# Kernel tuning notes

Hardware: AMD Instinct MI355X
Metric: run time of the kernel (lower is better)

The kernel has to match this reference:

```python
import jax, jax.numpy as jnp
import numpy as np

N_NODES = 50000
N_EDGES = 600000
D_IN, D_HID, D_OUT = 128, 256, 128


def setup_inputs() -> dict:
    key = jax.random.key(0)
    ks = jax.random.split(key, 8)
    x = jax.random.normal(ks[0], (N_NODES, D_IN), dtype=jnp.float32)
    edge_index = jax.random.randint(ks[1], (2, N_EDGES), 0, N_NODES, dtype=jnp.int64)
    # init_method='uniform' -> edge_weights initialized to ones
    edge_weights = jnp.ones((N_EDGES,), dtype=jnp.float32)
    def lin(k, din, dout):
        s = 1.0 / np.sqrt(din)
        return jax.random.uniform(k, (din, dout), jnp.float32, -s, s)
    W1 = lin(ks[2], D_IN, D_HID)
    b1 = jnp.zeros((D_HID,), jnp.float32)
    W2 = lin(ks[3], D_HID, D_HID)
    b2 = jnp.zeros((D_HID,), jnp.float32)
    W3 = lin(ks[4], D_HID, D_OUT)
    b3 = jnp.zeros((D_OUT,), jnp.float32)
    return {"x": x, "edge_index": edge_index, "edge_weights": edge_weights,
            "W1": W1, "b1": b1, "W2": W2, "b2": b2, "W3": W3, "b3": b3}


def reference(x, edge_index, edge_weights, W1, b1, W2, b2, W3, b3):
    N = x.shape[0]
    # learnable metric: softplus on raw edge weights
    ew = jax.nn.softplus(edge_weights)
    src, dst = edge_index[0], edge_index[1]
    # GCNConv default: add self-loops with weight 1.0
    loop = jnp.arange(N, dtype=edge_index.dtype)
    s = jnp.concatenate([src, loop])
    d = jnp.concatenate([dst, loop])
    w = jnp.concatenate([ew, jnp.ones((N,), ew.dtype)])
    # symmetric degree normalization (gcn_norm); identical edge_weight across layers
    deg = jax.ops.segment_sum(w, d, num_segments=N)
    dinv = jnp.where(deg > 0, jax.lax.rsqrt(deg), jnp.zeros_like(deg))
    norm = dinv[s] * w * dinv[d]  # [E+N]

    def gcn_conv(h, W, b):
        h = h @ W                              # [N, dout]
        msg = h[s] * norm[:, None]             # gather + scale: [E+N, dout]
        out = jax.ops.segment_sum(msg, d, num_segments=N)  # scatter-add
        return out + b

    h = jax.nn.relu(gcn_conv(x, W1, b1))   # dropout p=0.0 -> identity
    h = jax.nn.relu(gcn_conv(h, W2, b2))
    return gcn_conv(h, W3, b3)
```

## Files before the change

kernel.cpp:

```cpp
#include <hip/hip_runtime.h>
#include <hip/hip_fp16.h>
#include <math.h>

#define N_NODES 50000
#define N_EDGES 600000
#define D_IN    128
#define D_HID   256
#define D_OUT   128
#define NB_SCAN ((N_NODES + 255) / 256)

typedef unsigned short u16;
typedef __attribute__((ext_vector_type(8))) _Float16 f16x8;
typedef __attribute__((ext_vector_type(4))) float f32x4;

__device__ __forceinline__ u16 f2h(float x) {
    __half h = __float2half_rn(x);
    return *reinterpret_cast<u16*>(&h);
}
__device__ __forceinline__ float h2f(u16 h) {
    __half hh = *reinterpret_cast<__half*>(&h);
    return __half2float(hh);
}
__device__ __forceinline__ float2 h2f2(unsigned int raw) {
    __half2 h = *reinterpret_cast<__half2*>(&raw);
    return __half22float2(h);
}


__global__ void k_hist(const int* __restrict__ dst, const float* __restrict__ w,
                       float* __restrict__ ew, int* __restrict__ rank,
                       int* __restrict__ cnt) {
    int e = blockIdx.x * blockDim.x + threadIdx.x;
    if (e >= N_EDGES) return;
    float x = w[e];
    ew[e] = fmaxf(x, 0.f) + log1pf(expf(-fabsf(x)));
    rank[e] = atomicAdd(&cnt[dst[e]], 1);
}

__global__ void k_scan1(const int* __restrict__ cnt, int* __restrict__ rowptr,
                        int* __restrict__ bsum) {
    __shared__ int s[256];
    int b = blockIdx.x, t = threadIdx.x;
    int i = b * 256 + t;
    int v = (i < N_NODES) ? cnt[i] : 0;
    s[t] = v;
    __syncthreads();
    for (int off = 1; off < 256; off <<= 1) {
        int u = (t >= off) ? s[t - off] : 0;
        __syncthreads();
        s[t] += u;
        __syncthreads();
    }
    if (i < N_NODES) rowptr[i] = s[t] - v;
    if (t == 255) bsum[b] = s[255];
}

__global__ void k_scan2(const int* __restrict__ bsum, int* __restrict__ boff) {
    __shared__ int s[256];
    int t = threadIdx.x;
    int v = (t < NB_SCAN) ? bsum[t] : 0;
    s[t] = v;
    __syncthreads();
    for (int off = 1; off < 256; off <<= 1) {
        int u = (t >= off) ? s[t - off] : 0;
        __syncthreads();
        s[t] += u;
        __syncthreads();
    }
    if (t < NB_SCAN) boff[t] = s[t] - v;
    if (t == 255) boff[NB_SCAN] = s[255];
}

__global__ void k_scan3(int* __restrict__ rowptr, const int* __restrict__ boff) {
    int b = blockIdx.x, t = threadIdx.x;
    int i = b * 256 + t;
    if (i < N_NODES) rowptr[i] += boff[b];
    if (i == 0) rowptr[N_NODES] = boff[NB_SCAN];
}

__global__ void k_fill2(const int* __restrict__ src, const int* __restrict__ dst,
                        const float* __restrict__ ew, const int* __restrict__ rank,
                        const int* __restrict__ rowptr, int2* __restrict__ ecsr) {
    int e = blockIdx.x * blockDim.x + threadIdx.x;
    if (e >= N_EDGES) return;
    int pos = rowptr[dst[e]] + rank[e];
    ecsr[pos] = make_int2(src[e], __float_as_int(ew[e]));
}

__global__ void k_degdinv(const int* __restrict__ rowptr, const int2* __restrict__ ecsr,
                          float* __restrict__ dinv) {
    int n = blockIdx.x * blockDim.x + threadIdx.x;
    if (n >= N_NODES) return;
    int beg = rowptr[n], end = rowptr[n + 1];
    float s = 1.0f;
    for (int p = beg; p < end; p++) s += __int_as_float(ecsr[p].y);
    dinv[n] = rsqrtf(s);
}

__global__ void k_norm(const int* __restrict__ rowptr, const float* __restrict__ dinv,
                       int2* __restrict__ ecsr) {
    int n = blockIdx.x * blockDim.x + threadIdx.x;
    if (n >= N_NODES) return;
    int beg = rowptr[n], end = rowptr[n + 1];
    float dn = dinv[n];
    for (int p = beg; p < end; p++) {
        int2 r = ecsr[p];
        float w = dinv[r.x] * __int_as_float(r.y) * dn;
        ecsr[p] = make_int2(r.x, __float_as_int(w));
    }
}


#define WPREP_TOTAL 131072

__global__ void k_wprep(const float* __restrict__ W1, const float* __restrict__ W2,
                        const float* __restrict__ W3,
                        u16* __restrict__ B1, u16* __restrict__ B2, u16* __restrict__ B3) {
    int idx = blockIdx.x * blockDim.x + threadIdx.x;
    const float* W; u16* B; int K, N, base;
    if (idx < 32768)       { W = W1; B = B1; K = 128; N = 256; base = 0; }
    else if (idx < 98304)  { W = W2; B = B2; K = 256; N = 256; base = 32768; }
    else if (idx < 131072) { W = W3; B = B3; K = 256; N = 128; base = 98304; }
    else return;
    int p = idx - base;
    int n = p % N, k = p / N;
    float x = W[(size_t)k * N + n];
    u16 hi = f2h(x);
    u16 lo = f2h(x - h2f(hi));
    B[(size_t)n * (2 * K) + k] = hi;
    B[(size_t)n * (2 * K) + K + k] = lo;
}


template <int D, int INF, int OUTM, bool BIAS>
__global__ __launch_bounds__(256) void k_agg(const void* __restrict__ inv,
                                             const int* __restrict__ rowptr,
                                             const int2* __restrict__ ecsr,
                                             const float* __restrict__ dinv,
                                             const float* __restrict__ bias,
                                             void* __restrict__ outv) {
    int node = blockIdx.x * 4 + (threadIdx.x >> 6);
    int lane = threadIdx.x & 63;
    if (node >= N_NODES) return;
    float dn = dinv[node];
    float dd = dn * dn;
    int beg = rowptr[node], end = rowptr[node + 1];

    if (D == 256) {
        const float* inf = (const float*)inv;
        const u16* inh = (const u16*)inv;
        float sx, sy, sz, sw;
        if (INF == 0) {
            float4 sv = *(reinterpret_cast<const float4*>(inf + (size_t)node * D) + lane);
            sx = sv.x; sy = sv.y; sz = sv.z; sw = sv.w;
        } else {
            uint2 raw = *reinterpret_cast<const uint2*>(inh + (size_t)node * D + lane * 4);
            float2 f01 = h2f2(raw.x), f23 = h2f2(raw.y);
            sx = f01.x; sy = f01.y; sz = f23.x; sw = f23.y;
        }
        float ax = dd * sx, ay = dd * sy, az = dd * sz, aw = dd * sw;
        int p = beg;
        for (; p + 4 <= end; p += 4) {
            int2 e0 = ecsr[p], e1 = ecsr[p + 1], e2 = ecsr[p + 2], e3 = ecsr[p + 3];
            float w0 = __int_as_float(e0.y), w1 = __int_as_float(e1.y);
            float w2 = __int_as_float(e2.y), w3 = __int_as_float(e3.y);
            if (INF == 0) {
                float4 r0 = *(reinterpret_cast<const float4*>(inf + (size_t)e0.x * D) + lane);
                float4 r1 = *(reinterpret_cast<const float4*>(inf + (size_t)e1.x * D) + lane);
                float4 r2 = *(reinterpret_cast<const float4*>(inf + (size_t)e2.x * D) + lane);
                float4 r3 = *(reinterpret_cast<const float4*>(inf + (size_t)e3.x * D) + lane);
                ax += w0 * r0.x; ay += w0 * r0.y; az += w0 * r0.z; aw += w0 * r0.w;
                ax += w1 * r1.x; ay += w1 * r1.y; az += w1 * r1.z; aw += w1 * r1.w;
                ax += w2 * r2.x; ay += w2 * r2.y; az += w2 * r2.z; aw += w2 * r2.w;
                ax += w3 * r3.x; ay += w3 * r3.y; az += w3 * r3.z; aw += w3 * r3.w;
            } else {
                uint2 q0 = *reinterpret_cast<const uint2*>(inh + (size_t)e0.x * D + lane * 4);
                uint2 q1 = *reinterpret_cast<const uint2*>(inh + (size_t)e1.x * D + lane * 4);
                uint2 q2 = *reinterpret_cast<const uint2*>(inh + (size_t)e2.x * D + lane * 4);
                uint2 q3 = *reinterpret_cast<const uint2*>(inh + (size_t)e3.x * D + lane * 4);
                float2 a0 = h2f2(q0.x), b0 = h2f2(q0.y);
                float2 a1 = h2f2(q1.x), b1 = h2f2(q1.y);
                float2 a2 = h2f2(q2.x), b2 = h2f2(q2.y);
                float2 a3 = h2f2(q3.x), b3 = h2f2(q3.y);
                ax += w0 * a0.x; ay += w0 * a0.y; az += w0 * b0.x; aw += w0 * b0.y;
                ax += w1 * a1.x; ay += w1 * a1.y; az += w1 * b1.x; aw += w1 * b1.y;
                ax += w2 * a2.x; ay += w2 * a2.y; az += w2 * b2.x; aw += w2 * b2.y;
                ax += w3 * a3.x; ay += w3 * a3.y; az += w3 * b3.x; aw += w3 * b3.y;
            }
        }
        for (; p < end; p++) {
            int2 e0 = ecsr[p];
            float w0 = __int_as_float(e0.y);
            if (INF == 0) {
                float4 r0 = *(reinterpret_cast<const float4*>(inf + (size_t)e0.x * D) + lane);
                ax += w0 * r0.x; ay += w0 * r0.y; az += w0 * r0.z; aw += w0 * r0.w;
            } else {
                uint2 q0 = *reinterpret_cast<const uint2*>(inh + (size_t)e0.x * D + lane * 4);
                float2 a0 = h2f2(q0.x), b0 = h2f2(q0.y);
                ax += w0 * a0.x; ay += w0 * a0.y; az += w0 * b0.x; aw += w0 * b0.y;
            }
        }
        if (OUTM == 0) {
            float* out = (float*)outv;
            if (BIAS) {
                float4 b = *(reinterpret_cast<const float4*>(bias) + lane);
                ax += b.x; ay += b.y; az += b.z; aw += b.w;
            }
            float4 res; res.x = ax; res.y = ay; res.z = az; res.w = aw;
            *(reinterpret_cast<float4*>(out + (size_t)node * D) + lane) = res;
        } else {
            u16* out = (u16*)outv;
            ushort4 hv;
            hv.x = f2h(ax); hv.y = f2h(ay); hv.z = f2h(az); hv.w = f2h(aw);
            *reinterpret_cast<ushort4*>(out + (size_t)node * D + lane * 4) = hv;
        }
    } else {
        const float* inf = (const float*)inv;
        const u16* inh = (const u16*)inv;
        float sx, sy;
        if (INF == 0) {
            float2 sv = *(reinterpret_cast<const float2*>(inf + (size_t)node * D) + lane);
            sx = sv.x; sy = sv.y;
        } else {
            unsigned int raw = *reinterpret_cast<const unsigned int*>(inh + (size_t)node * D + lane * 2);
            float2 f = h2f2(raw);
            sx = f.x; sy = f.y;
        }
        float ax = dd * sx, ay = dd * sy;
        int p = beg;
        for (; p + 4 <= end; p += 4) {
            int2 e0 = ecsr[p], e1 = ecsr[p + 1], e2 = ecsr[p + 2], e3 = ecsr[p + 3];
            float w0 = __int_as_float(e0.y), w1 = __int_as_float(e1.y);
            float w2 = __int_as_float(e2.y), w3 = __int_as_float(e3.y);
            if (INF == 0) {
                float2 r0 = *(reinterpret_cast<const float2*>(inf + (size_t)e0.x * D) + lane);
                float2 r1 = *(reinterpret_cast<const float2*>(inf + (size_t)e1.x * D) + lane);
                float2 r2 = *(reinterpret_cast<const float2*>(inf + (size_t)e2.x * D) + lane);
                float2 r3 = *(reinterpret_cast<const float2*>(inf + (size_t)e3.x * D) + lane);
                ax += w0 * r0.x; ay += w0 * r0.y;
                ax += w1 * r1.x; ay += w1 * r1.y;
                ax += w2 * r2.x; ay += w2 * r2.y;
                ax += w3 * r3.x; ay += w3 * r3.y;
            } else {
                unsigned int q0 = *reinterpret_cast<const unsigned int*>(inh + (size_t)e0.x * D + lane * 2);
                unsigned int q1 = *reinterpret_cast<const unsigned int*>(inh + (size_t)e1.x * D + lane * 2);
                unsigned int q2 = *reinterpret_cast<const unsigned int*>(inh + (size_t)e2.x * D + lane * 2);
                unsigned int q3 = *reinterpret_cast<const unsigned int*>(inh + (size_t)e3.x * D + lane * 2);
                float2 f0 = h2f2(q0), f1 = h2f2(q1), f2 = h2f2(q2), f3 = h2f2(q3);
                ax += w0 * f0.x; ay += w0 * f0.y;
                ax += w1 * f1.x; ay += w1 * f1.y;
                ax += w2 * f2.x; ay += w2 * f2.y;
                ax += w3 * f3.x; ay += w3 * f3.y;
            }
        }
        for (; p < end; p++) {
            int2 e0 = ecsr[p];
            float w0 = __int_as_float(e0.y);
            if (INF == 0) {
                float2 r0 = *(reinterpret_cast<const float2*>(inf + (size_t)e0.x * D) + lane);
                ax += w0 * r0.x; ay += w0 * r0.y;
            } else {
                unsigned int q0 = *reinterpret_cast<const unsigned int*>(inh + (size_t)e0.x * D + lane * 2);
                float2 f0 = h2f2(q0);
                ax += w0 * f0.x; ay += w0 * f0.y;
            }
        }
        if (OUTM == 0) {
            float* out = (float*)outv;
            if (BIAS) {
                float2 b = *(reinterpret_cast<const float2*>(bias) + lane);
                ax += b.x; ay += b.y;
            }
            float2 res; res.x = ax; res.y = ay;
            *(reinterpret_cast<float2*>(out + (size_t)node * D) + lane) = res;
        } else {
            u16* out = (u16*)outv;
            ushort2 hv; hv.x = f2h(ax); hv.y = f2h(ay);
            *reinterpret_cast<ushort2*>(out + (size_t)node * D + lane * 2) = hv;
        }
    }
}


template <int OUT, bool BIAS, bool RELU>
__global__ __launch_bounds__(256) void k_gemm_h(const u16* __restrict__ Ap,
                                                const u16* __restrict__ Bp,
                                                const float* __restrict__ bias,
                                                void* __restrict__ Cv,
                                                int M, int K, int NN) {
    const int KP2 = 2 * K;
    __shared__ u16 As[8 * 544];
    __shared__ u16 Bs[2 * 8 * 544];
    int tid = threadIdx.x;
    int bm = blockIdx.y * 128;
    int bn = blockIdx.x * 128;
    int l = tid & 63;
    int w = tid >> 6;
    int wr = w >> 1, wc = w & 1;

    f32x4 zero = {0.f, 0.f, 0.f, 0.f};
    f32x4 acc[4][4];
    #pragma unroll
    for (int i = 0; i < 4; i++)
        #pragma unroll
        for (int j = 0; j < 4; j++) acc[i][j] = zero;

    for (int k0 = 0; k0 < K; k0 += 32) {
        #pragma unroll
        for (int q = 0; q < 2; q++) {
            int idx = tid + q * 256;
            int r = idx >> 2, o = idx & 3;
            int gr = bm + r;
            uint4 va = make_uint4(0u, 0u, 0u, 0u);
            if (gr < M)
                va = *reinterpret_cast<const uint4*>(Ap + (size_t)gr * K + k0 + o * 8);
            *reinterpret_cast<uint4*>(&As[(r >> 4) * 544 + o * 136 + (r & 15) * 8]) = va;
        }
        #pragma unroll
        for (int q = 0; q < 4; q++) {
            int idx = tid + q * 256;
            int r = idx >> 3, oct = idx & 7;
            int hf = oct >> 2, o = oct & 3;
            uint4 vb = *reinterpret_cast<const uint4*>(
                Bp + (size_t)(bn + r) * KP2 + hf * K + k0 + o * 8);
            *reinterpret_cast<uint4*>(
                &Bs[hf * 4352 + (r >> 4) * 544 + o * 136 + (r & 15) * 8]) = vb;
        }
        __syncthreads();
        int fro = (l >> 4) * 136 + (l & 15) * 8;
        f16x8 a[4], bh[4], bl[4];
        #pragma unroll
        for (int i = 0; i < 4; i++)
            a[i] = *reinterpret_cast<const f16x8*>(&As[(wr * 4 + i) * 544 + fro]);
        #pragma unroll
        for (int j = 0; j < 4; j++) {
            bh[j] = *reinterpret_cast<const f16x8*>(&Bs[(wc * 4 + j) * 544 + fro]);
            bl[j] = *reinterpret_cast<const f16x8*>(&Bs[4352 + (wc * 4 + j) * 544 + fro]);
        }
        #pragma unroll
        for (int i = 0; i < 4; i++)
            #pragma unroll
            for (int j = 0; j < 4; j++) {
                acc[i][j] = __builtin_amdgcn_mfma_f32_16x16x32_f16(a[i], bh[j], acc[i][j], 0, 0, 0);
                acc[i][j] = __builtin_amdgcn_mfma_f32_16x16x32_f16(a[i], bl[j], acc[i][j], 0, 0, 0);
            }
        __syncthreads();
    }

    int cl = l & 15;
    int rq = (l >> 4) * 4;
    float bv[4];
    #pragma unroll
    for (int j = 0; j < 4; j++) {
        int gc = bn + wc * 64 + j * 16 + cl;
        bv[j] = BIAS ? bias[gc] : 0.f;
    }
    #pragma unroll
    for (int i = 0; i < 4; i++) {
        #pragma unroll
        for (int r = 0; r < 4; r++) {
            int grow = bm + wr * 64 + i * 16 + rq + r;
            if (grow >= M) continue;
            #pragma unroll
            for (int j = 0; j < 4; j++) {
                int gc = bn + wc * 64 + j * 16 + cl;
                float v = acc[i][j][r];
                if (BIAS) v += bv[j];
                if (RELU) v = fmaxf(v, 0.f);
                if (OUT == 0) {
                    ((float*)Cv)[(size_t)grow * NN + gc] = v;
                } else {
                    ((u16*)Cv)[(size_t)grow * NN + gc] = f2h(v);
                }
            }
        }
    }
}


extern "C" void kernel_launch(void* const* d_in, const int* in_sizes, int n_in,
                              void* d_out, int out_size, void* d_ws, size_t ws_size,
                              hipStream_t stream) {
    const float* x   = (const float*)d_in[0];
    const int*   ei  = (const int*)d_in[1];
    const float* wts = (const float*)d_in[2];
    const float* W1  = (const float*)d_in[3];
    const float* b1  = (const float*)d_in[4];
    const float* W2  = (const float*)d_in[5];
    const float* b2  = (const float*)d_in[6];
    const float* W3  = (const float*)d_in[7];
    const float* b3  = (const float*)d_in[8];
    float* out = (float*)d_out;
    const int* src = ei;
    const int* dst = ei + N_EDGES;

    float* bufA   = (float*)d_ws;
    float* bufB   = bufA + (size_t)N_NODES * D_HID;
    float* ew     = bufB + (size_t)N_NODES * D_HID;
    float* dinv   = ew + N_EDGES;
    int*   cnt    = (int*)(dinv + N_NODES);
    int*   rank   = cnt + N_NODES;
    int*   rowptr = rank + N_EDGES;
    int2*  ecsr   = (int2*)(rowptr + (N_NODES + 2));
    u16*   Wb1    = (u16*)(ecsr + N_EDGES);
    u16*   Wb2    = Wb1 + 256 * 256;
    u16*   Wb3    = Wb2 + 256 * 512;
    int*   bsum   = (int*)(Wb3 + 128 * 512);
    int*   boff   = bsum + NB_SCAN;

    hipMemsetAsync(cnt, 0, sizeof(int) * N_NODES, stream);

    int ethreads = 256;
    int eblocks = (N_EDGES + ethreads - 1) / ethreads;
    int nblocks = (N_NODES + 255) / 256;
    k_hist<<<eblocks, ethreads, 0, stream>>>(dst, wts, ew, rank, cnt);
    k_scan1<<<NB_SCAN, 256, 0, stream>>>(cnt, rowptr, bsum);
    k_scan2<<<1, 256, 0, stream>>>(bsum, boff);
    k_scan3<<<NB_SCAN, 256, 0, stream>>>(rowptr, boff);
    k_fill2<<<eblocks, ethreads, 0, stream>>>(src, dst, ew, rank, rowptr, ecsr);
    k_degdinv<<<nblocks, 256, 0, stream>>>(rowptr, ecsr, dinv);
    k_norm<<<nblocks, 256, 0, stream>>>(rowptr, dinv, ecsr);
    k_wprep<<<(WPREP_TOTAL + 255) / 256, 256, 0, stream>>>(W1, W2, W3, Wb1, Wb2, Wb3);

    int aggBlocks = (N_NODES + 3) / 4;
    int gy = (N_NODES + 127) / 128;

    k_agg<128, 0, 1, false><<<aggBlocks, 256, 0, stream>>>(x, rowptr, ecsr, dinv, nullptr, bufA);
    {
        dim3 g(2, gy);
        k_gemm_h<1, true, true><<<g, 256, 0, stream>>>((const u16*)bufA, Wb1, b1, bufB,
                                                       N_NODES, D_IN, D_HID);
    }
    k_agg<256, 1, 1, false><<<aggBlocks, 256, 0, stream>>>(bufB, rowptr, ecsr, dinv, nullptr, bufA);
    {
        dim3 g(2, gy);
        k_gemm_h<1, true, true><<<g, 256, 0, stream>>>((const u16*)bufA, Wb2, b2, bufB,
                                                       N_NODES, D_HID, D_HID);
    }
    {
        dim3 g(1, gy);
        k_gemm_h<1, false, false><<<g, 256, 0, stream>>>((const u16*)bufB, Wb3, nullptr, bufA,
                                                         N_NODES, D_HID, D_OUT);
    }
    k_agg<128, 1, 0, true><<<aggBlocks, 256, 0, stream>>>(bufA, rowptr, ecsr, dinv, b3, out);
}
```

Before: 346.7 us.

## Sort CSR neighbors within each row by source chunk for gather locality

```diff
diff --git a/kernel.cpp b/kernel.cpp
--- a/kernel.cpp
+++ b/kernel.cpp
@@ -7,7 +7,11 @@
 #define D_IN    128
 #define D_HID   256
 #define D_OUT   128
-#define NB_SCAN ((N_NODES + 255) / 256)
+
+#define CSH   11
+#define NCH   ((N_NODES + (1 << CSH) - 1) >> CSH)
+#define NBINS (N_NODES * NCH)
+#define NB1   ((NBINS + 255) / 256)
 
 typedef unsigned short u16;
 typedef __attribute__((ext_vector_type(8))) _Float16 f16x8;
@@ -27,22 +31,23 @@
 }
 
 
-__global__ void k_hist(const int* __restrict__ dst, const float* __restrict__ w,
-                       float* __restrict__ ew, int* __restrict__ rank,
-                       int* __restrict__ cnt) {
+__global__ void k_hist(const int* __restrict__ src, const int* __restrict__ dst,
+                       const float* __restrict__ w, float* __restrict__ ew,
+                       int* __restrict__ rank, int* __restrict__ cnt2) {
     int e = blockIdx.x * blockDim.x + threadIdx.x;
     if (e >= N_EDGES) return;
     float x = w[e];
     ew[e] = fmaxf(x, 0.f) + log1pf(expf(-fabsf(x)));
-    rank[e] = atomicAdd(&cnt[dst[e]], 1);
-}
-
-__global__ void k_scan1(const int* __restrict__ cnt, int* __restrict__ rowptr,
+    int key = dst[e] * NCH + (src[e] >> CSH);
+    rank[e] = atomicAdd(&cnt2[key], 1);
+}
+
+__global__ void k_scan1(const int* __restrict__ cnt2, int* __restrict__ rowptr2,
                         int* __restrict__ bsum) {
     __shared__ int s[256];
     int b = blockIdx.x, t = threadIdx.x;
     int i = b * 256 + t;
-    int v = (i < N_NODES) ? cnt[i] : 0;
+    int v = (i < NBINS) ? cnt2[i] : 0;
     s[t] = v;
     __syncthreads();
     for (int off = 1; off < 256; off <<= 1) {
@@ -51,40 +56,56 @@
         s[t] += u;
         __syncthreads();
     }
-    if (i < N_NODES) rowptr[i] = s[t] - v;
+    if (i < NBINS) rowptr2[i] = s[t] - v;
     if (t == 255) bsum[b] = s[255];
 }
 
 __global__ void k_scan2(const int* __restrict__ bsum, int* __restrict__ boff) {
     __shared__ int s[256];
+    __shared__ int carry;
     int t = threadIdx.x;
-    int v = (t < NB_SCAN) ? bsum[t] : 0;
-    s[t] = v;
+    if (t == 0) carry = 0;
     __syncthreads();
-    for (int off = 1; off < 256; off <<= 1) {
-        int u = (t >= off) ? s[t - off] : 0;
-        __syncthreads();
-        s[t] += u;
-        __syncthreads();
-    }
-    if (t < NB_SCAN) boff[t] = s[t] - v;
-    if (t == 255) boff[NB_SCAN] = s[255];
-}
-
-__global__ void k_scan3(int* __restrict__ rowptr, const int* __restrict__ boff) {
+    for (int base = 0; base < NB1; base += 256) {
+        int i = base + t;
+        int v = (i < NB1) ? bsum[i] : 0;
+        s[t] = v;
+        __syncthreads();
+        for (int off = 1; off < 256; off <<= 1) {
+            int u = (t >= off) ? s[t - off] : 0;
+            __syncthreads();
+            s[t] += u;
+            __syncthreads();
+        }
+        if (i < NB1) boff[i] = carry + s[t] - v;
+        __syncthreads();
+        if (t == 255) carry += s[255];
+        __syncthreads();
+    }
+    if (t == 0) boff[NB1] = carry;
+}
+
+__global__ void k_scan3(int* __restrict__ rowptr2, const int* __restrict__ boff,
+                        int* __restrict__ rowptr) {
     int b = blockIdx.x, t = threadIdx.x;
     int i = b * 256 + t;
-    if (i < N_NODES) rowptr[i] += boff[b];
-    if (i == 0) rowptr[N_NODES] = boff[NB_SCAN];
+    if (i < NBINS) {
+        int v = rowptr2[i] + boff[b];
+        rowptr2[i] = v;
+        if (i % NCH == 0) rowptr[i / NCH] = v;
+    }
+    if (i == 0) rowptr[N_NODES] = boff[NB1];
 }
 
 __global__ void k_fill2(const int* __restrict__ src, const int* __restrict__ dst,
                         const float* __restrict__ ew, const int* __restrict__ rank,
-                        const int* __restrict__ rowptr, int2* __restrict__ ecsr) {
+                        const int* __restrict__ rowptr2, int2* __restrict__ ecsr) {
     int e = blockIdx.x * blockDim.x + threadIdx.x;
     if (e >= N_EDGES) return;
-    int pos = rowptr[dst[e]] + rank[e];
-    ecsr[pos] = make_int2(src[e], __float_as_int(ew[e]));
+    int s = src[e];
+    int key = dst[e] * NCH + (s >> CSH);
+    int pos = rowptr2[key] + rank[e];
+    ecsr[pos] = make_int2(s, __float_as_int(ew[e]));
 }
 
 __global__ void k_degdinv(const int* __restrict__ rowptr, const int2* __restrict__ ecsr,
@@ -394,30 +415,31 @@
     const int* src = ei;
     const int* dst = ei + N_EDGES;
 
-    float* bufA   = (float*)d_ws;
-    float* bufB   = bufA + (size_t)N_NODES * D_HID;
-    float* ew     = bufB + (size_t)N_NODES * D_HID;
-    float* dinv   = ew + N_EDGES;
-    int*   cnt    = (int*)(dinv + N_NODES);
-    int*   rank   = cnt + N_NODES;
-    int*   rowptr = rank + N_EDGES;
-    int2*  ecsr   = (int2*)(rowptr + (N_NODES + 2));
-    u16*   Wb1    = (u16*)(ecsr + N_EDGES);
-    u16*   Wb2    = Wb1 + 256 * 256;
-    u16*   Wb3    = Wb2 + 256 * 512;
-    int*   bsum   = (int*)(Wb3 + 128 * 512);
-    int*   boff   = bsum + NB_SCAN;
-
-    hipMemsetAsync(cnt, 0, sizeof(int) * N_NODES, stream);
+    float* bufA    = (float*)d_ws;
+    float* bufB    = bufA + (size_t)N_NODES * D_HID;
+    float* ew      = bufB + (size_t)N_NODES * D_HID;
+    float* dinv    = ew + N_EDGES;
+    int*   rank    = (int*)(dinv + N_NODES);
+    int*   rowptr  = rank + N_EDGES;
+    int2*  ecsr    = (int2*)(rowptr + (N_NODES + 2));
+    u16*   Wb1     = (u16*)(ecsr + N_EDGES);
+    u16*   Wb2     = Wb1 + 256 * 256;
+    u16*   Wb3     = Wb2 + 256 * 512;
+    int*   cnt2    = (int*)(Wb3 + 128 * 512);
+    int*   rowptr2 = cnt2 + NBINS;
+    int*   bsum    = rowptr2 + NBINS + 2;
+    int*   boff    = bsum + NB1;
+
+    hipMemsetAsync(cnt2, 0, sizeof(int) * NBINS, stream);
 
     int ethreads = 256;
     int eblocks = (N_EDGES + ethreads - 1) / ethreads;
     int nblocks = (N_NODES + 255) / 256;
-    k_hist<<<eblocks, ethreads, 0, stream>>>(dst, wts, ew, rank, cnt);
-    k_scan1<<<NB_SCAN, 256, 0, stream>>>(cnt, rowptr, bsum);
+    k_hist<<<eblocks, ethreads, 0, stream>>>(src, dst, wts, ew, rank, cnt2);
+    k_scan1<<<NB1, 256, 0, stream>>>(cnt2, rowptr2, bsum);
     k_scan2<<<1, 256, 0, stream>>>(bsum, boff);
-    k_scan3<<<NB_SCAN, 256, 0, stream>>>(rowptr, boff);
-    k_fill2<<<eblocks, ethreads, 0, stream>>>(src, dst, ew, rank, rowptr, ecsr);
+    k_scan3<<<NB1, 256, 0, stream>>>(rowptr2, boff, rowptr);
+    k_fill2<<<eblocks, ethreads, 0, stream>>>(src, dst, ew, rank, rowptr2, ecsr);
     k_degdinv<<<nblocks, 256, 0, stream>>>(rowptr, ecsr, dinv);
     k_norm<<<nblocks, 256, 0, stream>>>(rowptr, dinv, ecsr);
     k_wprep<<<(WPREP_TOTAL + 255) / 256, 256, 0, stream>>>(W1, W2, W3, Wb1, Wb2, Wb3);
```

New measurement: 380.9 us. +9.9%, slower.
